# Performance work log

Measured on AMD Instinct MI355X. Metric: run time of the kernel, lower is better.

The kernel has to match this reference:

```python
import jax, jax.numpy as jnp
import numpy as np

D_MODEL = 1024
NUM_HEADS = 16
DEPTH = D_MODEL // NUM_HEADS


def setup_inputs() -> dict:
    key = jax.random.key(0)
    ks = jax.random.split(key, 5)
    s = 1.0 / np.sqrt(D_MODEL)
    return {
        "x": jax.random.normal(ks[0], (4, 2048, D_MODEL), dtype=jnp.float32),
        "wq": jax.random.normal(ks[1], (D_MODEL, D_MODEL), dtype=jnp.float32) * s,
        "bq": jnp.zeros((D_MODEL,), dtype=jnp.float32),
        "wk": jax.random.normal(ks[2], (D_MODEL, D_MODEL), dtype=jnp.float32) * s,
        "bk": jnp.zeros((D_MODEL,), dtype=jnp.float32),
        "wv": jax.random.normal(ks[3], (D_MODEL, D_MODEL), dtype=jnp.float32) * s,
        "bv": jnp.zeros((D_MODEL,), dtype=jnp.float32),
        "wo": jax.random.normal(ks[4], (D_MODEL, D_MODEL), dtype=jnp.float32) * s,
        "bo": jnp.zeros((D_MODEL,), dtype=jnp.float32),
    }


def reference(x, wq, bq, wk, bk, wv, bv, wo, bo):
    B, S, _ = x.shape
    def split_heads(t):  # [B,S,D] -> [B,H,S,depth]
        return t.reshape(B, S, NUM_HEADS, DEPTH).transpose(0, 2, 1, 3)
    q = split_heads(x @ wq + bq)
    k = split_heads(x @ wk + bk)
    v = split_heads(x @ wv + bv)
    scale = 1.0 / jnp.sqrt(jnp.float32(DEPTH))
    logits = jnp.einsum("bhqd,bhkd->bhqk", q, k) * scale
    attn = jax.nn.softmax(logits, axis=-1)  # dropout is identity at inference
    out = jnp.einsum("bhqk,bhkd->bhqd", attn, v)
    out = out.transpose(0, 2, 1, 3).reshape(B, S, D_MODEL)
    return out @ wo + bo
```

## Files before the change

### kernel.cpp

```cpp
#include <hip/hip_runtime.h>
#include <hip/hip_bf16.h>
#include <cstdint>
#include <cstddef>

typedef __attribute__((ext_vector_type(8))) short s8v;
typedef __attribute__((ext_vector_type(4))) float f4v;
typedef __attribute__((ext_vector_type(16))) float f16v;
typedef __attribute__((ext_vector_type(4))) unsigned u4v;

#define MFMA_BF16(a, b, c) __builtin_amdgcn_mfma_f32_16x16x32_bf16((a), (b), (c), 0, 0, 0)
#define MFMA32(a, b, c) __builtin_amdgcn_mfma_f32_32x32x16_bf16((a), (b), (c), 0, 0, 0)

__device__ __forceinline__ short f2bf(float f) {
    unsigned u = __builtin_bit_cast(unsigned, f);
    u += 0x7FFFu + ((u >> 16) & 1u);
    return (short)(u >> 16);
}

__device__ __forceinline__ unsigned cvt_pk_bf16(float a, float b) {
    unsigned r;
    asm("v_cvt_pk_bf16_f32 %0, %1, %2" : "=v"(r) : "v"(a), "v"(b));
    return r;
}

#define GLDS16(gsrc, ldst)                                                                   \
    __builtin_amdgcn_global_load_lds(                                                        \
        (const __attribute__((address_space(1))) unsigned int*)(gsrc),                       \
        (__attribute__((address_space(3))) unsigned int*)(ldst), 16, 0, 0)

__global__ void convert_x(const float4* __restrict__ in, short4* __restrict__ out, int n4) {
    int i = blockIdx.x * blockDim.x + threadIdx.x;
    int stride = gridDim.x * blockDim.x;
    for (; i < n4; i += stride) {
        float4 v = in[i];
        short4 o;
        o.x = f2bf(v.x); o.y = f2bf(v.y); o.z = f2bf(v.z); o.w = f2bf(v.w);
        out[i] = o;
    }
}

__global__ void transpose_w(const float* __restrict__ a0, const float* __restrict__ a1,
                            const float* __restrict__ a2, const float* __restrict__ a3,
                            short* __restrict__ outb) {
    const float* src = (blockIdx.z == 0) ? a0 : (blockIdx.z == 1) ? a1 : (blockIdx.z == 2) ? a2 : a3;
    short* dst = outb + (size_t)blockIdx.z * 1048576;
    __shared__ float t[32][33];
    const int n0 = blockIdx.x * 32, k0 = blockIdx.y * 32;
    const int tid = threadIdx.x;
    const int rr = tid >> 3, c4 = (tid & 7) * 4;
    float4 v = *(const float4*)(src + (size_t)(k0 + rr) * 1024 + n0 + c4);
    t[rr][c4 + 0] = v.x; t[rr][c4 + 1] = v.y; t[rr][c4 + 2] = v.z; t[rr][c4 + 3] = v.w;
    __syncthreads();
    short4 o;
    o.x = f2bf(t[c4 + 0][rr]); o.y = f2bf(t[c4 + 1][rr]);
    o.z = f2bf(t[c4 + 2][rr]); o.w = f2bf(t[c4 + 3][rr]);
    *(short4*)(dst + (size_t)(n0 + rr) * 1024 + k0 + c4) = o;
}

template <typename OUT_T, int MODE>
__global__ __launch_bounds__(256, 2) void gemm_bt(const short* __restrict__ A,
                                                  const short* __restrict__ B,
                                                  const float* __restrict__ bias,
                                                  OUT_T* __restrict__ C,
                                                  int M, int N, int K, float alpha) {
    __shared__ short As[128 * 64];
    __shared__ short Bs[128 * 64];
    const int tid = threadIdx.x;
    const int lane = tid & 63;
    const int w = tid >> 6;
    const int wr = w >> 1, wc = w & 1;
    const int m0 = blockIdx.y * 128, n0 = blockIdx.x * 128;
    const int KB = K * 2;

    f4v acc[4][4] = {};

    for (int kt = 0; kt < K; kt += 64) {
#pragma unroll
        for (int i = 0; i < 4; i++) {
            int o = tid * 16 + i * 4096;
            int r = o >> 7;
            int cs = (o & 127) ^ ((r & 7) << 4);
            GLDS16((const char*)A + (size_t)(m0 + r) * KB + kt * 2 + cs,
                   (char*)As + (w * 1024 + i * 4096));
            GLDS16((const char*)B + (size_t)(n0 + r) * KB + kt * 2 + cs,
                   (char*)Bs + (w * 1024 + i * 4096));
        }
        __syncthreads();
#pragma unroll
        for (int kk = 0; kk < 2; kk++) {
            s8v af[4], bf[4];
#pragma unroll
            for (int mi = 0; mi < 4; mi++) {
                int r = wr * 64 + mi * 16 + (lane & 15);
                int cb = (((lane >> 4) * 16) + kk * 64) ^ ((r & 7) << 4);
                af[mi] = *(const s8v*)((const char*)As + r * 128 + cb);
            }
#pragma unroll
            for (int ni = 0; ni < 4; ni++) {
                int r = wc * 64 + ni * 16 + (lane & 15);
                int cb = (((lane >> 4) * 16) + kk * 64) ^ ((r & 7) << 4);
                bf[ni] = *(const s8v*)((const char*)Bs + r * 128 + cb);
            }
#pragma unroll
            for (int mi = 0; mi < 4; mi++)
#pragma unroll
                for (int ni = 0; ni < 4; ni++)
                    acc[mi][ni] = MFMA_BF16(af[mi], bf[ni], acc[mi][ni]);
        }
        __syncthreads();
    }

#pragma unroll
    for (int mi = 0; mi < 4; mi++) {
#pragma unroll
        for (int ni = 0; ni < 4; ni++) {
            int row = m0 + wr * 64 + mi * 16 + ((lane >> 4) << 2);
            int col = n0 + wc * 64 + ni * 16 + (lane & 15);
#pragma unroll
            for (int j = 0; j < 4; j++) {
                float v = acc[mi][ni][j];
                if constexpr (MODE == 0) {
                    v = (v + bias[col]) * alpha;
                    size_t idx = (size_t)(row + j) * N + col;
                    if constexpr (sizeof(OUT_T) == 2) C[idx] = (OUT_T)f2bf(v);
                    else C[idx] = v;
                } else {
                    v = (v + bias[row + j]) * alpha;
                    size_t idx = (size_t)(col >> 11) * (2048 * 1024) + (size_t)(row + j) * 2048 + (col & 2047);
                    C[idx] = (OUT_T)f2bf(v);
                }
            }
        }
    }
}

__global__ __launch_bounds__(256, 4) void attn_fwd(const short* __restrict__ Qb,
                                                   const short* __restrict__ Kb,
                                                   const short* __restrict__ Vtb,
                                                   short* __restrict__ AOb) {
    __shared__ short Ks[2][64 * 64];
    __shared__ short Vs[2][64 * 64];

    const int tid = threadIdx.x, lane = tid & 63, w = tid >> 6;
    const int l5 = lane & 31, H = lane >> 5;
    const int qt = blockIdx.x;
    const int bh = blockIdx.y;
    const int b = bh >> 4, h = bh & 15;
    const int q0 = qt * 128 + w * 32;

    s8v qf[4];
#pragma unroll
    for (int st = 0; st < 4; st++)
        qf[st] = *(const s8v*)(Qb + (size_t)(b * 2048 + q0 + l5) * 1024 + h * 64 + st * 16 + H * 8);

    f16v oacc[2] = {};
    float m_ = -1e30f, l_ = 0.f;

    auto STAGE = [&](int s0, int bi) {
#pragma unroll
        for (int i = 0; i < 2; i++) {
            int o = tid * 16 + i * 4096;
            int r = o >> 7;
            int cs = (o & 127) ^ ((r & 7) << 4);
            GLDS16((const char*)Kb + (size_t)(b * 2048 + s0 + r) * 2048 + h * 128 + cs,
                   (char*)Ks[bi] + w * 1024 + i * 4096);
            GLDS16((const char*)Vtb + (size_t)(b * 1024 + h * 64 + r) * 4096 + (size_t)s0 * 2 + cs,
                   (char*)Vs[bi] + w * 1024 + i * 4096);
        }
    };

    STAGE(0, 0);
    __syncthreads();

    int cur = 0;
    for (int t = 0; t < 32; t++) {
        if (t < 31) STAGE((t + 1) * 64, cur ^ 1);

        f16v sf[2] = {};
        __builtin_amdgcn_s_setprio(1);
#pragma unroll
        for (int kt = 0; kt < 2; kt++) {
            int r = kt * 32 + l5;
            int swz = (r & 7) << 4;
#pragma unroll
            for (int st = 0; st < 4; st++) {
                s8v kf = *(const s8v*)((const char*)Ks[cur] + r * 128 + ((st * 32 + H * 16) ^ swz));
                sf[kt] = MFMA32(kf, qf[st], sf[kt]);
            }
        }
        __builtin_amdgcn_s_setprio(0);

        float mx[16];
#pragma unroll
        for (int i = 0; i < 16; i++) mx[i] = fmaxf(sf[0][i], sf[1][i]);
#pragma unroll
        for (int stp = 8; stp >= 1; stp >>= 1)
#pragma unroll
            for (int i = 0; i < stp; i++) mx[i] = fmaxf(mx[i], mx[i + stp]);
        float tm = fmaxf(mx[0], __shfl_xor(mx[0], 32, 64));

        if (!__all(tm - m_ <= 8.0f)) {
            float mn = fmaxf(m_, tm);
            float fac = __builtin_amdgcn_exp2f(m_ - mn);
            m_ = mn;
            l_ *= fac;
#pragma unroll
            for (int dt = 0; dt < 2; dt++)
#pragma unroll
                for (int i = 0; i < 16; i++) oacc[dt][i] *= fac;
        }

        float rs0 = 0.f, rs1 = 0.f;
#pragma unroll
        for (int kt = 0; kt < 2; kt++)
#pragma unroll
            for (int i = 0; i < 16; i++) {
                float p = __builtin_amdgcn_exp2f(sf[kt][i] - m_);
                sf[kt][i] = p;
                if (i & 1) rs1 += p; else rs0 += p;
            }
        float rs = rs0 + rs1;
        rs += __shfl_xor(rs, 32, 64);
        l_ += rs;

#pragma unroll
        for (int s = 0; s < 4; s++) {
            const int kt = s >> 1, base = (s & 1) * 8;
            unsigned dA0 = cvt_pk_bf16(sf[kt][base + 0], sf[kt][base + 1]);
            unsigned dA1 = cvt_pk_bf16(sf[kt][base + 2], sf[kt][base + 3]);
            unsigned dB0 = cvt_pk_bf16(sf[kt][base + 4], sf[kt][base + 5]);
            unsigned dB1 = cvt_pk_bf16(sf[kt][base + 6], sf[kt][base + 7]);
            asm("v_permlane32_swap_b32 %0, %1" : "+v"(dA0), "+v"(dB0));
            asm("v_permlane32_swap_b32 %0, %1" : "+v"(dA1), "+v"(dB1));
            u4v fw = {dA0, dA1, dB0, dB1};
            s8v pfrag = __builtin_bit_cast(s8v, fw);
            __builtin_amdgcn_s_setprio(1);
#pragma unroll
            for (int dt = 0; dt < 2; dt++) {
                int r = dt * 32 + l5;
                s8v vf = *(const s8v*)((const char*)Vs[cur] + r * 128 + ((s * 32 + H * 16) ^ ((r & 7) << 4)));
                oacc[dt] = MFMA32(vf, pfrag, oacc[dt]);
            }
            __builtin_amdgcn_s_setprio(0);
        }
        __syncthreads();
        cur ^= 1;
    }

    float rl = 1.0f / l_;
    size_t orow = (size_t)(b * 2048 + q0 + l5) * 1024 + h * 64;
#pragma unroll
    for (int dt = 0; dt < 2; dt++)
#pragma unroll
        for (int g = 0; g < 4; g++) {
            short4 o;
            o.x = f2bf(oacc[dt][4 * g + 0] * rl);
            o.y = f2bf(oacc[dt][4 * g + 1] * rl);
            o.z = f2bf(oacc[dt][4 * g + 2] * rl);
            o.w = f2bf(oacc[dt][4 * g + 3] * rl);
            *(short4*)(AOb + orow + dt * 32 + g * 8 + H * 4) = o;
        }
}

extern "C" void kernel_launch(void* const* d_in, const int* in_sizes, int n_in,
                              void* d_out, int out_size, void* d_ws, size_t ws_size,
                              hipStream_t stream) {
    const float* x  = (const float*)d_in[0];
    const float* wq = (const float*)d_in[1];
    const float* bq = (const float*)d_in[2];
    const float* wk = (const float*)d_in[3];
    const float* bk = (const float*)d_in[4];
    const float* wv = (const float*)d_in[5];
    const float* bv = (const float*)d_in[6];
    const float* wo = (const float*)d_in[7];
    const float* bo = (const float*)d_in[8];
    float* out = (float*)d_out;

    char* ws = (char*)d_ws;
    const size_t MB16 = 16777216;
    short* xb  = (short*)(ws);
    short* qb  = (short*)(ws + 1 * MB16);
    short* kb  = (short*)(ws + 2 * MB16);
    short* vtb = (short*)(ws + 3 * MB16);
    short* wT  = (short*)(ws + 4 * MB16);
    short* aob = xb;

    const float qscale = 0.125f * 1.4426950408889634f;

    convert_x<<<dim3(1024), dim3(256), 0, stream>>>((const float4*)x, (short4*)xb, 8388608 / 4);
    transpose_w<<<dim3(32, 32, 4), dim3(256), 0, stream>>>(wq, wk, wv, wo, wT);

    gemm_bt<short, 0><<<dim3(8, 64), dim3(256), 0, stream>>>(xb, wT, bq, qb, 8192, 1024, 1024, qscale);
    gemm_bt<short, 0><<<dim3(8, 64), dim3(256), 0, stream>>>(xb, wT + 1048576, bk, kb, 8192, 1024, 1024, 1.0f);
    gemm_bt<short, 1><<<dim3(64, 8), dim3(256), 0, stream>>>(wT + 2 * 1048576, xb, bv, vtb, 1024, 8192, 1024, 1.0f);

    attn_fwd<<<dim3(16, 64), dim3(256), 0, stream>>>(qb, kb, vtb, aob);

    gemm_bt<float, 0><<<dim3(8, 64), dim3(256), 0, stream>>>(aob, wT + 3 * 1048576, bo, out, 8192, 1024, 1024, 1.0f);
}
```

Measured before the change: 211.8 us.

## Process two query groups per wave in attention to reuse K/V fragments

```diff
diff --git a/kernel.cpp b/kernel.cpp
--- a/kernel.cpp
+++ b/kernel.cpp
@@ -134,7 +134,7 @@
     }
 }
 
-__global__ __launch_bounds__(256, 4) void attn_fwd(const short* __restrict__ Qb,
+__global__ __launch_bounds__(256, 2) void attn_fwd(const short* __restrict__ Qb,
                                                    const short* __restrict__ Kb,
                                                    const short* __restrict__ Vtb,
                                                    short* __restrict__ AOb) {
@@ -146,22 +146,27 @@
     const int qt = blockIdx.x;
     const int bh = blockIdx.y;
     const int b = bh >> 4, h = bh & 15;
-    const int q0 = qt * 128 + w * 32;
-
-    s8v qf[4];
-#pragma unroll
-    for (int st = 0; st < 4; st++)
-        qf[st] = *(const s8v*)(Qb + (size_t)(b * 2048 + q0 + l5) * 1024 + h * 64 + st * 16 + H * 8);
-
-    f16v oacc[2] = {};
-    float m_ = -1e30f, l_ = 0.f;
+    const int q0 = qt * 256 + w * 64;
+
+    s8v qf[2][4];
+#pragma unroll
+    for (int g = 0; g < 2; g++)
+#pragma unroll
+        for (int st = 0; st < 4; st++)
+            qf[g][st] = *(const s8v*)(Qb + (size_t)(b * 2048 + q0 + g * 32 + l5) * 1024 +
+                                      h * 64 + st * 16 + H * 8);
+
+    f16v oacc[2][2] = {};
+    float m_[2] = {-1e30f, -1e30f};
+    float l_[2] = {0.f, 0.f};
 
     auto STAGE = [&](int s0, int bi) {
 #pragma unroll
         for (int i = 0; i < 2; i++) {
             int o = tid * 16 + i * 4096;
             int r = o >> 7;
-            int cs = (o & 127) ^ ((r & 7) << 4);
+            int px = (o & 127) ^ ((r & 7) << 4);
+            int cs = (px & 0x2F) | ((px & 16) << 2) | ((px & 64) >> 2);
             GLDS16((const char*)Kb + (size_t)(b * 2048 + s0 + r) * 2048 + h * 128 + cs,
                    (char*)Ks[bi] + w * 1024 + i * 4096);
             GLDS16((const char*)Vtb + (size_t)(b * 1024 + h * 64 + r) * 4096 + (size_t)s0 * 2 + cs,
@@ -176,7 +181,7 @@
     for (int t = 0; t < 32; t++) {
         if (t < 31) STAGE((t + 1) * 64, cur ^ 1);
 
-        f16v sf[2] = {};
+        f16v sf[2][2] = {};
         __builtin_amdgcn_s_setprio(1);
 #pragma unroll
         for (int kt = 0; kt < 2; kt++) {
@@ -184,62 +189,75 @@
             int swz = (r & 7) << 4;
 #pragma unroll
             for (int st = 0; st < 4; st++) {
-                s8v kf = *(const s8v*)((const char*)Ks[cur] + r * 128 + ((st * 32 + H * 16) ^ swz));
-                sf[kt] = MFMA32(kf, qf[st], sf[kt]);
+                int col = (H << 6) | ((st & 1) << 5) | ((st >> 1) << 4);
+                s8v kf = *(const s8v*)((const char*)Ks[cur] + r * 128 + (col ^ swz));
+#pragma unroll
+                for (int g = 0; g < 2; g++)
+                    sf[g][kt] = MFMA32(kf, qf[g][st], sf[g][kt]);
             }
         }
         __builtin_amdgcn_s_setprio(0);
 
-        float mx[16];
-#pragma unroll
-        for (int i = 0; i < 16; i++) mx[i] = fmaxf(sf[0][i], sf[1][i]);
-#pragma unroll
-        for (int stp = 8; stp >= 1; stp >>= 1)
-#pragma unroll
-            for (int i = 0; i < stp; i++) mx[i] = fmaxf(mx[i], mx[i + stp]);
-        float tm = fmaxf(mx[0], __shfl_xor(mx[0], 32, 64));
-
-        if (!__all(tm - m_ <= 8.0f)) {
-            float mn = fmaxf(m_, tm);
-            float fac = __builtin_amdgcn_exp2f(m_ - mn);
-            m_ = mn;
-            l_ *= fac;
-#pragma unroll
-            for (int dt = 0; dt < 2; dt++)
-#pragma unroll
-                for (int i = 0; i < 16; i++) oacc[dt][i] *= fac;
-        }
-
-        float rs0 = 0.f, rs1 = 0.f;
-#pragma unroll
-        for (int kt = 0; kt < 2; kt++)
-#pragma unroll
-            for (int i = 0; i < 16; i++) {
-                float p = __builtin_amdgcn_exp2f(sf[kt][i] - m_);
-                sf[kt][i] = p;
-                if (i & 1) rs1 += p; else rs0 += p;
-            }
-        float rs = rs0 + rs1;
-        rs += __shfl_xor(rs, 32, 64);
-        l_ += rs;
+#pragma unroll
+        for (int g = 0; g < 2; g++) {
+            float mx[16];
+#pragma unroll
+            for (int i = 0; i < 16; i++) mx[i] = fmaxf(sf[g][0][i], sf[g][1][i]);
+#pragma unroll
+            for (int stp = 8; stp >= 1; stp >>= 1)
+#pragma unroll
+                for (int i = 0; i < stp; i++) mx[i] = fmaxf(mx[i], mx[i + stp]);
+            float tm = fmaxf(mx[0], __shfl_xor(mx[0], 32, 64));
+
+            if (!__all(tm - m_[g] <= 8.0f)) {
+                float mn = fmaxf(m_[g], tm);
+                float fac = __builtin_amdgcn_exp2f(m_[g] - mn);
+                m_[g] = mn;
+                l_[g] *= fac;
+#pragma unroll
+                for (int dt = 0; dt < 2; dt++)
+#pragma unroll
+                    for (int i = 0; i < 16; i++) oacc[g][dt][i] *= fac;
+            }
+
+            float rs0 = 0.f, rs1 = 0.f;
+#pragma unroll
+            for (int kt = 0; kt < 2; kt++)
+#pragma unroll
+                for (int i = 0; i < 16; i++) {
+                    float p = __builtin_amdgcn_exp2f(sf[g][kt][i] - m_[g]);
+                    sf[g][kt][i] = p;
+                    if (i & 1) rs1 += p; else rs0 += p;
+                }
+            float rs = rs0 + rs1;
+            rs += __shfl_xor(rs, 32, 64);
+            l_[g] += rs;
+        }
 
 #pragma unroll
         for (int s = 0; s < 4; s++) {
             const int kt = s >> 1, base = (s & 1) * 8;
-            unsigned dA0 = cvt_pk_bf16(sf[kt][base + 0], sf[kt][base + 1]);
-            unsigned dA1 = cvt_pk_bf16(sf[kt][base + 2], sf[kt][base + 3]);
-            unsigned dB0 = cvt_pk_bf16(sf[kt][base + 4], sf[kt][base + 5]);
-            unsigned dB1 = cvt_pk_bf16(sf[kt][base + 6], sf[kt][base + 7]);
-            asm("v_permlane32_swap_b32 %0, %1" : "+v"(dA0), "+v"(dB0));
-            asm("v_permlane32_swap_b32 %0, %1" : "+v"(dA1), "+v"(dB1));
-            u4v fw = {dA0, dA1, dB0, dB1};
-            s8v pfrag = __builtin_bit_cast(s8v, fw);
+            s8v pfrag[2];
+#pragma unroll
+            for (int g = 0; g < 2; g++) {
+                unsigned dA0 = cvt_pk_bf16(sf[g][kt][base + 0], sf[g][kt][base + 1]);
+                unsigned dA1 = cvt_pk_bf16(sf[g][kt][base + 2], sf[g][kt][base + 3]);
+                unsigned dB0 = cvt_pk_bf16(sf[g][kt][base + 4], sf[g][kt][base + 5]);
+                unsigned dB1 = cvt_pk_bf16(sf[g][kt][base + 6], sf[g][kt][base + 7]);
+                asm("v_permlane32_swap_b32 %0, %1" : "+v"(dA0), "+v"(dB0));
+                asm("v_permlane32_swap_b32 %0, %1" : "+v"(dA1), "+v"(dB1));
+                u4v fw = {dA0, dA1, dB0, dB1};
+                pfrag[g] = __builtin_bit_cast(s8v, fw);
+            }
             __builtin_amdgcn_s_setprio(1);
 #pragma unroll
             for (int dt = 0; dt < 2; dt++) {
                 int r = dt * 32 + l5;
-                s8v vf = *(const s8v*)((const char*)Vs[cur] + r * 128 + ((s * 32 + H * 16) ^ ((r & 7) << 4)));
-                oacc[dt] = MFMA32(vf, pfrag, oacc[dt]);
+                int col = (H << 6) | ((s & 1) << 5) | ((s >> 1) << 4);
+                s8v vf = *(const s8v*)((const char*)Vs[cur] + r * 128 + (col ^ ((r & 7) << 4)));
+#pragma unroll
+                for (int g = 0; g < 2; g++)
+                    oacc[g][dt] = MFMA32(vf, pfrag[g], oacc[g][dt]);
             }
             __builtin_amdgcn_s_setprio(0);
         }
@@ -247,19 +265,22 @@
         cur ^= 1;
     }
 
-    float rl = 1.0f / l_;
-    size_t orow = (size_t)(b * 2048 + q0 + l5) * 1024 + h * 64;
-#pragma unroll
-    for (int dt = 0; dt < 2; dt++)
-#pragma unroll
-        for (int g = 0; g < 4; g++) {
-            short4 o;
-            o.x = f2bf(oacc[dt][4 * g + 0] * rl);
-            o.y = f2bf(oacc[dt][4 * g + 1] * rl);
-            o.z = f2bf(oacc[dt][4 * g + 2] * rl);
-            o.w = f2bf(oacc[dt][4 * g + 3] * rl);
-            *(short4*)(AOb + orow + dt * 32 + g * 8 + H * 4) = o;
-        }
+#pragma unroll
+    for (int g = 0; g < 2; g++) {
+        float rl = 1.0f / l_[g];
+        size_t orow = (size_t)(b * 2048 + q0 + g * 32 + l5) * 1024 + h * 64;
+#pragma unroll
+        for (int dt = 0; dt < 2; dt++)
+#pragma unroll
+            for (int grp = 0; grp < 4; grp++) {
+                short4 o;
+                o.x = f2bf(oacc[g][dt][4 * grp + 0] * rl);
+                o.y = f2bf(oacc[g][dt][4 * grp + 1] * rl);
+                o.z = f2bf(oacc[g][dt][4 * grp + 2] * rl);
+                o.w = f2bf(oacc[g][dt][4 * grp + 3] * rl);
+                *(short4*)(AOb + orow + dt * 32 + grp * 8 + H * 4) = o;
+            }
+    }
 }
 
 extern "C" void kernel_launch(void* const* d_in, const int* in_sizes, int n_in,
@@ -294,7 +315,7 @@
     gemm_bt<short, 0><<<dim3(8, 64), dim3(256), 0, stream>>>(xb, wT + 1048576, bk, kb, 8192, 1024, 1024, 1.0f);
     gemm_bt<short, 1><<<dim3(64, 8), dim3(256), 0, stream>>>(wT + 2 * 1048576, xb, bv, vtb, 1024, 8192, 1024, 1.0f);
 
-    attn_fwd<<<dim3(16, 64), dim3(256), 0, stream>>>(qb, kb, vtb, aob);
+    attn_fwd<<<dim3(8, 64), dim3(256), 0, stream>>>(qb, kb, vtb, aob);
 
     gemm_bt<float, 0><<<dim3(8, 64), dim3(256), 0, stream>>>(aob, wT + 3 * 1048576, bo, out, 8192, 1024, 1024, 1.0f);
 }
```

Result: no change. 211.8 us (+0.0%).
